# Optimization experiments

Measured on AMD Instinct MI355X. Metric: run time of the kernel, lower is better.

## Reference

```python
import jax, jax.numpy as jnp
import numpy as np

OUT_SL = 32


def gru_cell(x, h, Wih, Whh, bih, bhh):
    # PyTorch GRU cell: gates ordered (r, z, n)
    gi = x @ Wih.T + bih
    gh = h @ Whh.T + bhh
    ir, iz, inn = jnp.split(gi, 3, axis=-1)
    hr, hz, hn = jnp.split(gh, 3, axis=-1)
    r = jax.nn.sigmoid(ir + hr)
    z = jax.nn.sigmoid(iz + hz)
    n = jnp.tanh(inn + r * hn)
    return (1.0 - z) * n + z * h


def run_gru_layer(xs, h0, Wih, Whh, bih, bhh, reverse=False):
    def step(h, x):
        h = gru_cell(x, h, Wih, Whh, bih, bhh)
        return h, h
    hT, ys = jax.lax.scan(step, h0, xs, reverse=reverse)
    return ys, hT


def setup_inputs() -> dict:
    key = jax.random.key(0)
    ks = iter(jax.random.split(key, 32))

    def p(shape, fan_in):
        return (jax.random.normal(next(ks), shape, dtype=jnp.float32)
                / np.sqrt(fan_in).astype(np.float32))

    V_ENC, V_DEC, EE, ED, NH = 32000, 32000, 300, 300, 256
    inp = jax.random.randint(next(ks), (128, 64), 0, V_ENC)
    return {
        'emb_enc': p((V_ENC, EE), 1.0),
        'enc_Wih0': p((2, 3 * NH, EE), EE),
        'enc_Whh0': p((2, 3 * NH, NH), NH),
        'enc_bih0': p((2, 3 * NH), NH),
        'enc_bhh0': p((2, 3 * NH), NH),
        'enc_Wih1': p((2, 3 * NH, 2 * NH), 2 * NH),
        'enc_Whh1': p((2, 3 * NH, NH), NH),
        'enc_bih1': p((2, 3 * NH), NH),
        'enc_bhh1': p((2, 3 * NH), NH),
        'W_out_enc': p((ED, 2 * NH), 2 * NH),
        'emb_dec': p((V_DEC, ED), 1.0),
        'dec_Wih': p((2, 3 * ED, ED), ED),
        'dec_Whh': p((2, 3 * ED, ED), ED),
        'dec_bih': p((2, 3 * ED), ED),
        'dec_bhh': p((2, 3 * ED), ED),
        'W1': p((2 * NH, ED), 2 * NH),
        'l2_W': p((ED, ED), ED),
        'l2_b': p((ED,), ED),
        'l3_W': p((ED, ED + 2 * NH), ED + 2 * NH),
        'l3_b': p((ED,), ED),
        'V_att': p((ED,), ED),
        'out_b': p((V_DEC,), ED),
        'inp': inp,
    }


def reference(emb_enc, enc_Wih0, enc_Whh0, enc_bih0, enc_bhh0,
              enc_Wih1, enc_Whh1, enc_bih1, enc_bhh1, W_out_enc,
              emb_dec, dec_Wih, dec_Whh, dec_bih, dec_bhh,
              W1, l2_W, l2_b, l3_W, l3_b, V_att, out_b, inp):
    sl, bs = inp.shape
    nh = enc_Whh0.shape[-1]
    h0 = jnp.zeros((bs, nh), dtype=emb_enc.dtype)

    # ---- encoder: 2-layer bidirectional GRU (dropout in eval mode = identity)
    emb = emb_enc[inp]                                        # (sl, bs, EE)
    yf0, hf0 = run_gru_layer(emb, h0, enc_Wih0[0], enc_Whh0[0], enc_bih0[0], enc_bhh0[0])
    yb0, hb0 = run_gru_layer(emb, h0, enc_Wih0[1], enc_Whh0[1], enc_bih0[1], enc_bhh0[1], reverse=True)
    x1 = jnp.concatenate([yf0, yb0], axis=-1)                 # (sl, bs, 2*nh)
    yf1, hf1 = run_gru_layer(x1, h0, enc_Wih1[0], enc_Whh1[0], enc_bih1[0], enc_bhh1[0])
    yb1, hb1 = run_gru_layer(x1, h0, enc_Wih1[1], enc_Whh1[1], enc_bih1[1], enc_bhh1[1], reverse=True)
    enc_out = jnp.concatenate([yf1, yb1], axis=-1)            # (sl, bs, 2*nh)

    # h.view(2,2,bs,-1).permute(0,2,1,3) -> concat fwd/bwd per layer
    h = jnp.stack([jnp.concatenate([hf0, hb0], axis=-1),
                   jnp.concatenate([hf1, hb1], axis=-1)])     # (2, bs, 2*nh)
    h = h @ W_out_enc.T                                       # (2, bs, ED)

    w1e = enc_out @ W1                                        # (sl, bs, ED)
    dec_inp0 = jnp.zeros((bs,), dtype=jnp.int32)

    def dec_step(carry, _):
        h, dec_inp = carry
        w2h = h[-1] @ l2_W.T + l2_b                           # (bs, ED)
        u = jnp.tanh(w1e + w2h[None])                         # (sl, bs, ED)
        a = jax.nn.softmax(u @ V_att, axis=0)                 # (sl, bs), softmax over seq
        Xa = jnp.einsum('sb,sbd->bd', a, enc_out)             # (bs, 2*nh)
        e = emb_dec[dec_inp]                                  # (bs, ED)
        x = jnp.concatenate([e, Xa], axis=1) @ l3_W.T + l3_b  # (bs, ED)
        h0n = gru_cell(x, h[0], dec_Wih[0], dec_Whh[0], dec_bih[0], dec_bhh[0])
        h1n = gru_cell(h0n, h[1], dec_Wih[1], dec_Whh[1], dec_bih[1], dec_bhh[1])
        outp = h1n @ emb_dec.T + out_b                        # (bs, V_dec), tied weights
        ndec = jnp.argmax(outp, axis=1).astype(jnp.int32)
        return (jnp.stack([h0n, h1n]), ndec), outp

    (_, _), res = jax.lax.scan(dec_step, (h, dec_inp0), None, length=OUT_SL)
    return res                                                # (out_sl, bs, V_dec)
```

## Files before the change

### kernel.cpp

```cpp
#include <hip/hip_runtime.h>
#include <math.h>


typedef unsigned long long ull;
typedef float v2f __attribute__((ext_vector_type(2)));

#define DINL static __device__ __forceinline__

DINL float sigm(float x) { return 1.0f / (1.0f + expf(-x)); }
DINL float dot4f(float4 a, float4 b) { return a.x*b.x + a.y*b.y + a.z*b.z + a.w*b.w; }

DINL ull packmax(float x, int v) {
  unsigned u = __float_as_uint(x);
  u = (u & 0x80000000u) ? ~u : (u | 0x80000000u);
  return ((ull)u << 32) | (unsigned)(~v);
}
DINL ull umax64(ull a, ull b) { return a > b ? a : b; }

DINL float atl(const float* p) {
  unsigned u = __hip_atomic_load((const unsigned*)p, __ATOMIC_RELAXED,
                                 __HIP_MEMORY_SCOPE_AGENT);
  return __uint_as_float(u);
}
DINL void atsf(float* p, float v) {
  __hip_atomic_exchange((unsigned*)p, __float_as_uint(v), __ATOMIC_RELAXED,
                        __HIP_MEMORY_SCOPE_AGENT);
}
DINL ull atl64(const ull* p) {
  return __hip_atomic_load(p, __ATOMIC_RELAXED, __HIP_MEMORY_SCOPE_AGENT);
}
DINL void ats64(ull* p, ull v) {
  __hip_atomic_exchange(p, v, __ATOMIC_RELAXED, __HIP_MEMORY_SCOPE_AGENT);
}

DINL void gbar(unsigned* flags, int wg, unsigned target, int tid) {
  asm volatile("s_waitcnt vmcnt(0)" ::: "memory");
  __syncthreads();
  if (tid == 0)
    __hip_atomic_exchange(&flags[wg * 32], target, __ATOMIC_RELAXED,
                          __HIP_MEMORY_SCOPE_AGENT);
  while (__hip_atomic_load(&flags[tid * 32], __ATOMIC_RELAXED,
                           __HIP_MEMORY_SCOPE_AGENT) < target)
    __builtin_amdgcn_s_sleep(1);
  __syncthreads();
}

__global__ __launch_bounds__(256) void k_embed(const float4* __restrict__ E,
                                               const int* __restrict__ inp,
                                               float4* __restrict__ out) {
  int i = blockIdx.x * 256 + threadIdx.x;
  if (i >= 8192 * 75) return;
  int row = i / 75, q = i - row * 75;
  out[i] = E[(size_t)inp[row] * 75 + q];
}

__global__ __launch_bounds__(256) void k_transpose(const float* __restrict__ A,
                                                   float* __restrict__ B, int R, int C) {
  __shared__ float tile[32][33];
  int c0 = blockIdx.x * 32, r0 = blockIdx.y * 32;
  int tx = threadIdx.x & 31, ty = threadIdx.x >> 5;
  for (int i = 0; i < 32; i += 8) {
    int r = r0 + ty + i, c = c0 + tx;
    if (r < R && c < C) tile[ty + i][tx] = A[(size_t)r * C + c];
  }
  __syncthreads();
  for (int i = 0; i < 32; i += 8) {
    int c = c0 + ty + i, r = r0 + tx;
    if (c < C && r < R) B[(size_t)c * R + r] = tile[tx][ty + i];
  }
}

__global__ __launch_bounds__(256) void k_packW(const float* __restrict__ Whh,
                                               float* __restrict__ W2) {
  int i = blockIdx.x * 256 + threadIdx.x;
  if (i >= 196608) return;
  int d = i / 98304, r = i - d * 98304, kp = r / 768, gc = r - kp * 768;
  const float* src = Whh + (size_t)d * 196608 + (size_t)gc * 256 + kp * 2;
  float* dst = W2 + (size_t)i * 2;
  dst[0] = src[0];
  dst[1] = src[1];
}

__global__ __launch_bounds__(256) void k_gemm128(const float* __restrict__ A,
                                                 const float* __restrict__ B,
                                                 const float* __restrict__ bias,
                                                 float* __restrict__ C,
                                                 int N, int M, int K) {
  __shared__ float As[8][132];
  __shared__ float Bs[8][132];
  const int tid = threadIdx.x;
  const int bn = blockIdx.x * 128, bm = blockIdx.y * 128;
  const int tn = (tid >> 4) << 3, tm = (tid & 15) << 3;
  const int r = tid & 127;
  const bool isB = tid >= 128;
  const float* src = isB ? (B + (size_t)(bm + r) * K) : (A + (size_t)(bn + r) * K);
  const bool rowok = isB ? (bm + r < M) : (bn + r < N);
  float acc[8][8] = {};
  for (int k0 = 0; k0 < K; k0 += 8) {
    float v[8];
    if (rowok && k0 + 8 <= K) {
      float4 p0 = *(const float4*)(src + k0);
      float4 p1 = *(const float4*)(src + k0 + 4);
      v[0]=p0.x; v[1]=p0.y; v[2]=p0.z; v[3]=p0.w;
      v[4]=p1.x; v[5]=p1.y; v[6]=p1.z; v[7]=p1.w;
    } else {
#pragma unroll
      for (int j = 0; j < 8; ++j) v[j] = (rowok && k0 + j < K) ? src[k0 + j] : 0.0f;
    }
    float (*dst)[132] = isB ? Bs : As;
#pragma unroll
    for (int j = 0; j < 8; ++j) dst[j][r] = v[j];
    __syncthreads();
#pragma unroll
    for (int kk = 0; kk < 8; ++kk) {
      float a[8], b[8];
      *(float4*)&a[0] = *(const float4*)&As[kk][tn];
      *(float4*)&a[4] = *(const float4*)&As[kk][tn + 4];
      *(float4*)&b[0] = *(const float4*)&Bs[kk][tm];
      *(float4*)&b[4] = *(const float4*)&Bs[kk][tm + 4];
#pragma unroll
      for (int i = 0; i < 8; ++i)
#pragma unroll
        for (int j = 0; j < 8; ++j) acc[i][j] += a[i] * b[j];
    }
    __syncthreads();
  }
#pragma unroll
  for (int i = 0; i < 8; ++i) {
    int row = bn + tn + i;
    if (row >= N) continue;
#pragma unroll
    for (int j = 0; j < 8; ++j) {
      int col = bm + tm + j;
      if (col < M) C[(size_t)row * M + col] = acc[i][j] + (bias ? bias[col] : 0.0f);
    }
  }
}

__global__ __launch_bounds__(256) void k_enc_rec(
    const float* __restrict__ giF, const float* __restrict__ giB,
    const float* __restrict__ W2,
    const float* __restrict__ bhh,
    float* __restrict__ y) {
  const int b0 = blockIdx.x * 2;
  const int dir = blockIdx.y;
  const int c = threadIdx.x;
  const float* gi = dir ? giB : giF;
  const v2f* Wv = (const v2f*)(W2 + (size_t)dir * 196608);
  const float* bh = bhh + dir * 768;

  __shared__ __align__(16) float hls[2][2][258];
  for (int i = c; i < 2 * 2 * 258; i += 256) ((float*)hls)[i] = 0.0f;
  __syncthreads();

  const float bhr = bh[c], bhz = bh[256 + c], bhn = bh[512 + c];

  const int tt0 = dir ? 127 : 0;
  const float* g0p = gi + (size_t)tt0 * 49152 + (size_t)b0 * 768;
  float g0r = g0p[c], g0z = g0p[256 + c], g0n = g0p[512 + c];
  float g1r = g0p[768 + c], g1z = g0p[1024 + c], g1n = g0p[1280 + c];

  for (int t = 0; t < 128; ++t) {
    const int cu = t & 1;
    float p0r = 0, p0z = 0, p0n = 0, p1r = 0, p1z = 0, p1n = 0;
    if (t < 127) {
      const int tn_ = dir ? 126 - t : t + 1;
      const float* gp = gi + (size_t)tn_ * 49152 + (size_t)b0 * 768;
      p0r = gp[c]; p0z = gp[256 + c]; p0n = gp[512 + c];
      p1r = gp[768 + c]; p1z = gp[1024 + c]; p1n = gp[1280 + c];
    }
    v2f a0r = {0,0}, a0z = {0,0}, a0n = {0,0};
    v2f a1r = {0,0}, a1z = {0,0}, a1n = {0,0};
    const float* h0p = &hls[cu][0][0];
    const float* h1p = &hls[cu][1][0];
#pragma unroll 4
    for (int kp = 0; kp < 128; ++kp) {
      v2f wr = Wv[kp * 768 + c];
      v2f wz = Wv[kp * 768 + 256 + c];
      v2f wn = Wv[kp * 768 + 512 + c];
      v2f h0 = *(const v2f*)&h0p[kp * 2];
      v2f h1 = *(const v2f*)&h1p[kp * 2];
      a0r += h0 * wr; a0z += h0 * wz; a0n += h0 * wn;
      a1r += h1 * wr; a1z += h1 * wz; a1n += h1 * wn;
    }
    float r0 = sigm(g0r + a0r.x + a0r.y + bhr);
    float z0 = sigm(g0z + a0z.x + a0z.y + bhz);
    float n0 = tanhf(g0n + r0 * (a0n.x + a0n.y + bhn));
    float h0new = (1.f - z0) * n0 + z0 * h0p[c];
    float r1 = sigm(g1r + a1r.x + a1r.y + bhr);
    float z1 = sigm(g1z + a1z.x + a1z.y + bhz);
    float n1 = tanhf(g1n + r1 * (a1n.x + a1n.y + bhn));
    float h1new = (1.f - z1) * n1 + z1 * h1p[c];
    hls[cu ^ 1][0][c] = h0new;
    hls[cu ^ 1][1][c] = h1new;
    const int tw = dir ? 127 - t : t;
    float* yp = y + (size_t)tw * 32768 + (size_t)b0 * 512 + dir * 256 + c;
    yp[0] = h0new;
    yp[512] = h1new;
    g0r = p0r; g0z = p0z; g0n = p0n; g1r = p1r; g1z = p1z; g1n = p1n;
    __syncthreads();
  }
}

__global__ __launch_bounds__(256) void k_hcat(const float* __restrict__ x1,
                                              const float* __restrict__ encout,
                                              float* __restrict__ hcat) {
  int i = blockIdx.x * 256 + threadIdx.x;
  int l = i >> 15, r = i & 32767, b = r >> 9, d = r & 511;
  const float* src = l ? encout : x1;
  int ts = (d < 256) ? 127 : 0;
  hcat[i] = src[((size_t)(ts << 6) + b) * 512 + d];
}

DINL void gru_at(int cb, int tid, const float* __restrict__ xin,
                 const float* __restrict__ hin, float* __restrict__ hout,
                 float* __restrict__ houtT,
                 const float* __restrict__ Wih, const float* __restrict__ Whh,
                 const float* __restrict__ bih, const float* __restrict__ bhh,
                 float* xs, float* hs) {
  const int cchunk = cb % 19, bchunk = cb / 19;
  const int cl = tid & 15, bl = tid >> 4;
  const int c = cchunk * 16 + cl;
  const int b0 = bchunk * 16, bq = b0 + bl;
  for (int i = tid; i < 4800; i += 256) {
    int row = i / 300, q = i - row * 300;
    xs[i] = atl(xin + (size_t)(b0 + row) * 300 + q);
    hs[i] = atl(hin + (size_t)(b0 + row) * 300 + q);
  }
  __syncthreads();
  if (c < 300) {
    float gir = bih[c], giz = bih[300 + c], gin = bih[600 + c];
    float ghr = bhh[c], ghz = bhh[300 + c], ghn = bhh[600 + c];
    const float4* wir = (const float4*)(Wih + (size_t)c * 300);
    const float4* wiz = (const float4*)(Wih + (size_t)(300 + c) * 300);
    const float4* win = (const float4*)(Wih + (size_t)(600 + c) * 300);
    const float4* whr = (const float4*)(Whh + (size_t)c * 300);
    const float4* whz = (const float4*)(Whh + (size_t)(300 + c) * 300);
    const float4* whn = (const float4*)(Whh + (size_t)(600 + c) * 300);
    const float4* xr = (const float4*)(xs + bl * 300);
    const float4* hr = (const float4*)(hs + bl * 300);
    for (int q = 0; q < 75; ++q) {
      float4 xv = xr[q], hv = hr[q];
      gir += dot4f(xv, wir[q]);
      giz += dot4f(xv, wiz[q]);
      gin += dot4f(xv, win[q]);
      ghr += dot4f(hv, whr[q]);
      ghz += dot4f(hv, whz[q]);
      ghn += dot4f(hv, whn[q]);
    }
    float r = sigm(gir + ghr), z = sigm(giz + ghz);
    float n = tanhf(gin + r * ghn);
    float hnew = (1.f - z) * n + z * hs[bl * 300 + c];
    atsf(&hout[(size_t)bq * 300 + c], hnew);
    if (houtT) atsf(&houtT[(size_t)c * 64 + bq], hnew);
  }
}

__global__ __launch_bounds__(256) void k_dec_all(
    float* __restrict__ dech, float* __restrict__ h1T, float* __restrict__ xdec,
    ull* __restrict__ bests, unsigned* __restrict__ flags,
    const float* __restrict__ w1e, const float* __restrict__ encout,
    const float* __restrict__ l2W, const float* __restrict__ l2b,
    const float* __restrict__ l3W, const float* __restrict__ l3b,
    const float* __restrict__ Vatt, const float* __restrict__ embdec,
    const float* __restrict__ dWih, const float* __restrict__ dWhh,
    const float* __restrict__ dbih, const float* __restrict__ dbhh,
    const float* __restrict__ embT, const float* __restrict__ outb,
    float* __restrict__ out) {
  const int wg = blockIdx.x, tid = threadIdx.x;
  __shared__ __align__(16) float smem[14400];
  unsigned tgt = 0;

  for (int t = 0; t < 32; ++t) {
    const int cur = t & 1;
    float* hc = dech + cur * 38400;
    float* hn = dech + (cur ^ 1) * 38400;

    if (wg < 64) {
      const int b = wg;
      float* h1s = smem;
      float* w2h = smem + 304;
      float* eXa = smem + 608;
      float* aa  = smem + 1424;
      float* red = smem + 1552;
      ull* redb  = (ull*)(smem + 1680);

      redb[tid] = (t > 0 && tid < 250) ? atl64(&bests[(size_t)tid * 64 + b]) : 0ULL;
      for (int i = tid; i < 300; i += 256) h1s[i] = atl(hc + 19200 + b * 300 + i);
      __syncthreads();
      for (int s = 128; s > 0; s >>= 1) {
        if (tid < s) redb[tid] = umax64(redb[tid], redb[tid + s]);
        __syncthreads();
      }
      const int ib = (t > 0) ? (int)(~(unsigned)(redb[0] & 0xFFFFFFFFULL)) : 0;

      for (int m = tid; m < 300; m += 256) {
        const float4* wr = (const float4*)(l2W + (size_t)m * 300);
        const float4* hr = (const float4*)h1s;
        float acc = l2b[m];
        for (int q = 0; q < 75; ++q) acc += dot4f(wr[q], hr[q]);
        w2h[m] = acc;
      }
      __syncthreads();

      if (tid < 128) {
        const float4* wp = (const float4*)(w1e + ((size_t)(tid << 6) + b) * 300);
        const float4* vp = (const float4*)Vatt;
        const float4* hp = (const float4*)w2h;
        float acc = 0.f;
        for (int q = 0; q < 75; ++q) {
          float4 w = wp[q], h = hp[q], v = vp[q];
          acc += tanhf(w.x + h.x) * v.x + tanhf(w.y + h.y) * v.y +
                 tanhf(w.z + h.z) * v.z + tanhf(w.w + h.w) * v.w;
        }
        aa[tid] = acc;
        red[tid] = acc;
      }
      __syncthreads();
      for (int s = 64; s > 0; s >>= 1) {
        if (tid < s) red[tid] = fmaxf(red[tid], red[tid + s]);
        __syncthreads();
      }
      float mx = red[0];
      __syncthreads();
      if (tid < 128) {
        float ex = expf(aa[tid] - mx);
        aa[tid] = ex;
        red[tid] = ex;
      }
      __syncthreads();
      for (int s = 64; s > 0; s >>= 1) {
        if (tid < s) red[tid] += red[tid + s];
        __syncthreads();
      }
      float inv = 1.0f / red[0];
      __syncthreads();
      if (tid < 128) aa[tid] *= inv;
      for (int d = tid; d < 300; d += 256) eXa[d] = embdec[(size_t)ib * 300 + d];
      __syncthreads();

      for (int d = tid; d < 512; d += 256) {
        float acc = 0.f;
        for (int s = 0; s < 128; ++s)
          acc += aa[s] * encout[((size_t)(s << 6) + b) * 512 + d];
        eXa[300 + d] = acc;
      }
      __syncthreads();

      for (int m = tid; m < 300; m += 256) {
        const float4* wr = (const float4*)(l3W + (size_t)m * 812);
        const float4* xr = (const float4*)eXa;
        float acc = l3b[m];
        for (int q = 0; q < 203; ++q) acc += dot4f(wr[q], xr[q]);
        atsf(&xdec[b * 300 + m], acc);
      }
    }
    gbar(flags, wg, ++tgt, tid);

    if (wg < 76)
      gru_at(wg, tid, xdec, hc, hn, nullptr, dWih, dWhh, dbih, dbhh,
             smem, smem + 4800);
    gbar(flags, wg, ++tgt, tid);

    if (wg < 76)
      gru_at(wg, tid, hn, hc + 19200, hn + 19200, h1T,
             dWih + 270000, dWhh + 270000, dbih + 900, dbhh + 900,
             smem, smem + 4800);
    gbar(flags, wg, ++tgt, tid);

    if (wg < 250) {
      const int v0 = wg * 128;
      const int vq = tid & 31, bo = tid >> 5;
      float acc[8][4];
#pragma unroll
      for (int i = 0; i < 8; ++i)
#pragma unroll
        for (int j = 0; j < 4; ++j) acc[i][j] = 0.f;
      float* hch = smem;
      float* et  = smem + 4800;
      for (int kc = 0; kc < 4; ++kc) {
        __syncthreads();
        for (int i = tid; i < 4800; i += 256) hch[i] = atl(h1T + kc * 4800 + i);
        for (int i = tid; i < 2400; i += 256) {
          int row = i >> 5, c4 = (i & 31) << 2;
          *(float4*)&et[(row << 7) + c4] =
              *(const float4*)(embT + (size_t)(kc * 75 + row) * 32000 + v0 + c4);
        }
        __syncthreads();
        for (int k = 0; k < 75; ++k) {
          float hv[8];
          *(float4*)&hv[0] = *(const float4*)&hch[(k << 6) + (bo << 3)];
          *(float4*)&hv[4] = *(const float4*)&hch[(k << 6) + (bo << 3) + 4];
          float4 ev = *(const float4*)&et[(k << 7) + (vq << 2)];
#pragma unroll
          for (int i = 0; i < 8; ++i) {
            acc[i][0] += hv[i] * ev.x;
            acc[i][1] += hv[i] * ev.y;
            acc[i][2] += hv[i] * ev.z;
            acc[i][3] += hv[i] * ev.w;
          }
        }
      }
      float4 bo4 = *(const float4*)(outb + v0 + (vq << 2));
      float* outp = out + (size_t)t * 2048000;
      float* sacc = smem;
      __syncthreads();
#pragma unroll
      for (int i = 0; i < 8; ++i) {
        const int b = (bo << 3) + i;
        float4 r;
        r.x = acc[i][0] + bo4.x; r.y = acc[i][1] + bo4.y;
        r.z = acc[i][2] + bo4.z; r.w = acc[i][3] + bo4.w;
        *(float4*)(outp + (size_t)b * 32000 + v0 + (vq << 2)) = r;
        sacc[((vq << 2) + 0) * 64 + b] = r.x;
        sacc[((vq << 2) + 1) * 64 + b] = r.y;
        sacc[((vq << 2) + 2) * 64 + b] = r.z;
        sacc[((vq << 2) + 3) * 64 + b] = r.w;
      }
      __syncthreads();
      if (tid < 64) {
        ull best = 0ULL;
#pragma unroll 4
        for (int v = 0; v < 128; ++v)
          best = umax64(best, packmax(sacc[v * 64 + tid], v0 + v));
        ats64(&bests[(size_t)wg * 64 + tid], best);
      }
    }
    if (t < 31) gbar(flags, wg, ++tgt, tid);
  }
}

extern "C" void kernel_launch(void* const* d_in, const int* in_sizes, int n_in,
                              void* d_out_v, int out_size, void* d_ws, size_t ws_size,
                              hipStream_t stream) {
  (void)in_sizes; (void)n_in; (void)out_size; (void)ws_size;
  const float* emb_enc = (const float*)d_in[0];
  const float* eWih0   = (const float*)d_in[1];
  const float* eWhh0   = (const float*)d_in[2];
  const float* ebih0   = (const float*)d_in[3];
  const float* ebhh0   = (const float*)d_in[4];
  const float* eWih1   = (const float*)d_in[5];
  const float* eWhh1   = (const float*)d_in[6];
  const float* ebih1   = (const float*)d_in[7];
  const float* ebhh1   = (const float*)d_in[8];
  const float* Wout    = (const float*)d_in[9];
  const float* emb_dec = (const float*)d_in[10];
  const float* dWih    = (const float*)d_in[11];
  const float* dWhh    = (const float*)d_in[12];
  const float* dbih    = (const float*)d_in[13];
  const float* dbhh    = (const float*)d_in[14];
  const float* W1      = (const float*)d_in[15];
  const float* l2W     = (const float*)d_in[16];
  const float* l2b     = (const float*)d_in[17];
  const float* l3W     = (const float*)d_in[18];
  const float* l3b     = (const float*)d_in[19];
  const float* Vatt    = (const float*)d_in[20];
  const float* outb    = (const float*)d_in[21];
  const int* inp       = (const int*)d_in[22];
  float* d_out = (float*)d_out_v;

  float* ws = (float*)d_ws;
  size_t off = 0;
  auto take = [&](size_t n) { float* p = ws + off; off += (n + 3) & ~(size_t)3; return p; };
  float* embT   = take((size_t)300 * 32000);
  float* encout = take((size_t)8192 * 512);
  float* w1e    = take((size_t)8192 * 300);
  float* W1T    = take((size_t)300 * 512);
  float* hcat   = take((size_t)128 * 512);
  float* dech   = take((size_t)2 * 2 * 64 * 300);
  float* h1T    = take((size_t)300 * 64);
  float* xdec   = take((size_t)64 * 300);
  ull* bests    = (ull*)take((size_t)250 * 64 * 2);
  unsigned* flags = (unsigned*)take((size_t)256 * 32);

  float* emb  = d_out;
  float* gi0f = emb + 2457600;
  float* gi0b = gi0f + 6291456;
  float* x1   = gi0b + 6291456;
  float* gi1f = x1 + 4194304;
  float* gi1b = gi1f + 6291456;
  float* W2L0 = d_out + 33554432;
  float* W2L1 = W2L0 + 393216;

  hipMemsetAsync(flags, 0, 256 * 32 * sizeof(unsigned), stream);

  k_embed<<<2400, 256, 0, stream>>>((const float4*)emb_enc, inp, (float4*)emb);
  k_transpose<<<dim3(10, 16), 256, 0, stream>>>(W1, W1T, 512, 300);
  k_transpose<<<dim3(10, 1000), 256, 0, stream>>>(emb_dec, embT, 32000, 300);
  k_packW<<<768, 256, 0, stream>>>(eWhh0, W2L0);
  k_packW<<<768, 256, 0, stream>>>(eWhh1, W2L1);

  k_gemm128<<<dim3(64, 6), 256, 0, stream>>>(emb, eWih0, ebih0, gi0f, 8192, 768, 300);
  k_gemm128<<<dim3(64, 6), 256, 0, stream>>>(emb, eWih0 + 230400, ebih0 + 768, gi0b, 8192, 768, 300);
  k_enc_rec<<<dim3(32, 2), 256, 0, stream>>>(gi0f, gi0b, W2L0, ebhh0, x1);

  k_gemm128<<<dim3(64, 6), 256, 0, stream>>>(x1, eWih1, ebih1, gi1f, 8192, 768, 512);
  k_gemm128<<<dim3(64, 6), 256, 0, stream>>>(x1, eWih1 + 393216, ebih1 + 768, gi1b, 8192, 768, 512);
  k_enc_rec<<<dim3(32, 2), 256, 0, stream>>>(gi1f, gi1b, W2L1, ebhh1, encout);

  k_hcat<<<256, 256, 0, stream>>>(x1, encout, hcat);
  k_gemm128<<<dim3(1, 3), 256, 0, stream>>>(hcat, Wout, nullptr, dech, 128, 300, 512);
  k_gemm128<<<dim3(64, 3), 256, 0, stream>>>(encout, W1T, nullptr, w1e, 8192, 300, 512);

  k_dec_all<<<256, 256, 0, stream>>>(dech, h1T, xdec, bests, flags,
                                     w1e, encout, l2W, l2b, l3W, l3b,
                                     Vatt, emb_dec, dWih, dWhh, dbih, dbhh,
                                     embT, outb, d_out);
}
```

Baseline: 11.03 ms.

## Cache decoder GRU weights in LDS per block and use atomic-counter grid barrier

The persistent decoder kernel now assigns the two GRU cells to disjoint block groups (0-75 and 76-151). Each block loads its 96-row slice of the GRU weights and biases into shared memory once, so weights are no longer re-read from global memory every step. The per-block flag barrier is replaced by one atomic counter that thread 0 polls, and the bests reduction is halved. The vocab projection now reads embT directly from global instead of staging it in LDS, and the argmax scratch is padded to avoid bank conflicts. Costs include a large LDS footprint that limits occupancy and contention on a single atomic counter.

```diff
diff --git a/kernel.cpp b/kernel.cpp
--- a/kernel.cpp
+++ b/kernel.cpp
@@ -33,15 +33,14 @@
   __hip_atomic_exchange(p, v, __ATOMIC_RELAXED, __HIP_MEMORY_SCOPE_AGENT);
 }
 
-DINL void gbar(unsigned* flags, int wg, unsigned target, int tid) {
+DINL void gbar(unsigned* cnt, unsigned target, int tid) {
   asm volatile("s_waitcnt vmcnt(0)" ::: "memory");
   __syncthreads();
-  if (tid == 0)
-    __hip_atomic_exchange(&flags[wg * 32], target, __ATOMIC_RELAXED,
-                          __HIP_MEMORY_SCOPE_AGENT);
-  while (__hip_atomic_load(&flags[tid * 32], __ATOMIC_RELAXED,
-                           __HIP_MEMORY_SCOPE_AGENT) < target)
-    __builtin_amdgcn_s_sleep(1);
+  if (tid == 0) {
+    __hip_atomic_fetch_add(cnt, 1u, __ATOMIC_RELAXED, __HIP_MEMORY_SCOPE_AGENT);
+    while (__hip_atomic_load(cnt, __ATOMIC_RELAXED, __HIP_MEMORY_SCOPE_AGENT) < target)
+      __builtin_amdgcn_s_sleep(4);
+  }
   __syncthreads();
 }
 
@@ -139,8 +138,7 @@
 
 __global__ __launch_bounds__(256) void k_enc_rec(
     const float* __restrict__ giF, const float* __restrict__ giB,
-    const float* __restrict__ W2,
-    const float* __restrict__ bhh,
+    const float* __restrict__ W2, const float* __restrict__ bhh,
     float* __restrict__ y) {
   const int b0 = blockIdx.x * 2;
   const int dir = blockIdx.y;
@@ -154,7 +152,6 @@
   __syncthreads();
 
   const float bhr = bh[c], bhz = bh[256 + c], bhn = bh[512 + c];
-
   const int tt0 = dir ? 127 : 0;
   const float* g0p = gi + (size_t)tt0 * 49152 + (size_t)b0 * 768;
   float g0r = g0p[c], g0z = g0p[256 + c], g0n = g0p[512 + c];
@@ -212,41 +209,40 @@
   hcat[i] = src[((size_t)(ts << 6) + b) * 512 + d];
 }
 
-DINL void gru_at(int cb, int tid, const float* __restrict__ xin,
-                 const float* __restrict__ hin, float* __restrict__ hout,
-                 float* __restrict__ houtT,
-                 const float* __restrict__ Wih, const float* __restrict__ Whh,
-                 const float* __restrict__ bih, const float* __restrict__ bhh,
-                 float* xs, float* hs) {
-  const int cchunk = cb % 19, bchunk = cb / 19;
-  const int cl = tid & 15, bl = tid >> 4;
-  const int c = cchunk * 16 + cl;
-  const int b0 = bchunk * 16, bq = b0 + bl;
+DINL void gru_lds(int cch, int bch, int tid,
+                  const float* __restrict__ xin, const float* __restrict__ hin,
+                  float* __restrict__ hout, float* __restrict__ houtT,
+                  const float* Wg, const float* biass, float* scr) {
+  float* xs = scr;
+  float* hs = scr + 4800;
+  const int b0 = bch * 16;
   for (int i = tid; i < 4800; i += 256) {
     int row = i / 300, q = i - row * 300;
     xs[i] = atl(xin + (size_t)(b0 + row) * 300 + q);
     hs[i] = atl(hin + (size_t)(b0 + row) * 300 + q);
   }
   __syncthreads();
+  const int cl = tid & 15, bl = tid >> 4;
+  const int c = cch * 16 + cl, bq = b0 + bl;
   if (c < 300) {
-    float gir = bih[c], giz = bih[300 + c], gin = bih[600 + c];
-    float ghr = bhh[c], ghz = bhh[300 + c], ghn = bhh[600 + c];
-    const float4* wir = (const float4*)(Wih + (size_t)c * 300);
-    const float4* wiz = (const float4*)(Wih + (size_t)(300 + c) * 300);
-    const float4* win = (const float4*)(Wih + (size_t)(600 + c) * 300);
-    const float4* whr = (const float4*)(Whh + (size_t)c * 300);
-    const float4* whz = (const float4*)(Whh + (size_t)(300 + c) * 300);
-    const float4* whn = (const float4*)(Whh + (size_t)(600 + c) * 300);
+    float gir = biass[cl],      giz = biass[16 + cl], gin = biass[32 + cl];
+    float ghr = biass[48 + cl], ghz = biass[64 + cl], ghn = biass[80 + cl];
     const float4* xr = (const float4*)(xs + bl * 300);
     const float4* hr = (const float4*)(hs + bl * 300);
+    const float4* w0 = (const float4*)(Wg + (0 * 16 + cl) * 308);
+    const float4* w1 = (const float4*)(Wg + (1 * 16 + cl) * 308);
+    const float4* w2 = (const float4*)(Wg + (2 * 16 + cl) * 308);
+    const float4* w3 = (const float4*)(Wg + (3 * 16 + cl) * 308);
+    const float4* w4 = (const float4*)(Wg + (4 * 16 + cl) * 308);
+    const float4* w5 = (const float4*)(Wg + (5 * 16 + cl) * 308);
     for (int q = 0; q < 75; ++q) {
       float4 xv = xr[q], hv = hr[q];
-      gir += dot4f(xv, wir[q]);
-      giz += dot4f(xv, wiz[q]);
-      gin += dot4f(xv, win[q]);
-      ghr += dot4f(hv, whr[q]);
-      ghz += dot4f(hv, whz[q]);
-      ghn += dot4f(hv, whn[q]);
+      gir += dot4f(xv, w0[q]);
+      giz += dot4f(xv, w1[q]);
+      gin += dot4f(xv, w2[q]);
+      ghr += dot4f(hv, w3[q]);
+      ghz += dot4f(hv, w4[q]);
+      ghn += dot4f(hv, w5[q]);
     }
     float r = sigm(gir + ghr), z = sigm(giz + ghz);
     float n = tanhf(gin + r * ghn);
@@ -254,11 +250,12 @@
     atsf(&hout[(size_t)bq * 300 + c], hnew);
     if (houtT) atsf(&houtT[(size_t)c * 64 + bq], hnew);
   }
+  __syncthreads();
 }
 
 __global__ __launch_bounds__(256) void k_dec_all(
     float* __restrict__ dech, float* __restrict__ h1T, float* __restrict__ xdec,
-    ull* __restrict__ bests, unsigned* __restrict__ flags,
+    ull* __restrict__ bests, unsigned* __restrict__ cnt,
     const float* __restrict__ w1e, const float* __restrict__ encout,
     const float* __restrict__ l2W, const float* __restrict__ l2b,
     const float* __restrict__ l3W, const float* __restrict__ l3b,
@@ -268,9 +265,41 @@
     const float* __restrict__ embT, const float* __restrict__ outb,
     float* __restrict__ out) {
   const int wg = blockIdx.x, tid = threadIdx.x;
-  __shared__ __align__(16) float smem[14400];
+  __shared__ __align__(16) float Wg[6 * 16 * 308];
+  __shared__ __align__(16) float scr[9600];
+  __shared__ float biass[96];
+
+  int grole = -1, gcell = 0;
+  if (wg < 76) { grole = wg; gcell = 0; }
+  else if (wg < 152) { grole = wg - 76; gcell = 1; }
+  const int cch = (grole >= 0) ? grole % 19 : 0;
+  const int bch = (grole >= 0) ? grole / 19 : 0;
+  if (grole >= 0) {
+    const float* Wih = dWih + gcell * 270000;
+    const float* Whh = dWhh + gcell * 270000;
+    for (int i = tid; i < 96 * 300; i += 256) {
+      int r = i / 300, k = i - r * 300;
+      int g = r >> 4, cl = r & 15;
+      int c = cch * 16 + cl;
+      float v = 0.f;
+      if (c < 300)
+        v = (g < 3) ? Wih[(size_t)(g * 300 + c) * 300 + k]
+                    : Whh[(size_t)((g - 3) * 300 + c) * 300 + k];
+      Wg[(g * 16 + cl) * 308 + k] = v;
+    }
+    if (tid < 96) {
+      int g = tid >> 4, cl = tid & 15;
+      int c = cch * 16 + cl;
+      float v = 0.f;
+      if (c < 300)
+        v = (g < 3) ? dbih[gcell * 900 + g * 300 + c]
+                    : dbhh[gcell * 900 + (g - 3) * 300 + c];
+      biass[tid] = v;
+    }
+  }
+  __syncthreads();
+
   unsigned tgt = 0;
-
   for (int t = 0; t < 32; ++t) {
     const int cur = t & 1;
     float* hc = dech + cur * 38400;
@@ -278,17 +307,24 @@
 
     if (wg < 64) {
       const int b = wg;
-      float* h1s = smem;
-      float* w2h = smem + 304;
-      float* eXa = smem + 608;
-      float* aa  = smem + 1424;
-      float* red = smem + 1552;
-      ull* redb  = (ull*)(smem + 1680);
-
-      redb[tid] = (t > 0 && tid < 250) ? atl64(&bests[(size_t)tid * 64 + b]) : 0ULL;
+      float* h1s = scr;
+      float* w2h = scr + 304;
+      float* eXa = scr + 608;
+      float* aa  = scr + 1424;
+      float* red = scr + 1552;
+      ull* redb  = (ull*)(scr + 1680);
+
+      if (tid < 128) {
+        ull m = 0ULL;
+        if (t > 0) {
+          m = atl64(&bests[(size_t)tid * 64 + b]);
+          if (tid + 128 < 250) m = umax64(m, atl64(&bests[(size_t)(tid + 128) * 64 + b]));
+        }
+        redb[tid] = m;
+      }
       for (int i = tid; i < 300; i += 256) h1s[i] = atl(hc + 19200 + b * 300 + i);
       __syncthreads();
-      for (int s = 128; s > 0; s >>= 1) {
+      for (int s = 64; s > 0; s >>= 1) {
         if (tid < s) redb[tid] = umax64(redb[tid], redb[tid + s]);
         __syncthreads();
       }
@@ -354,19 +390,17 @@
         for (int q = 0; q < 203; ++q) acc += dot4f(wr[q], xr[q]);
         atsf(&xdec[b * 300 + m], acc);
       }
-    }
-    gbar(flags, wg, ++tgt, tid);
+      __syncthreads();
+    }
+    gbar(cnt, 256u * (++tgt), tid);
 
     if (wg < 76)
-      gru_at(wg, tid, xdec, hc, hn, nullptr, dWih, dWhh, dbih, dbhh,
-             smem, smem + 4800);
-    gbar(flags, wg, ++tgt, tid);
-
-    if (wg < 76)
-      gru_at(wg, tid, hn, hc + 19200, hn + 19200, h1T,
-             dWih + 270000, dWhh + 270000, dbih + 900, dbhh + 900,
-             smem, smem + 4800);
-    gbar(flags, wg, ++tgt, tid);
+      gru_lds(cch, bch, tid, xdec, hc, hn, nullptr, Wg, biass, scr);
+    gbar(cnt, 256u * (++tgt), tid);
+
+    if (wg >= 76 && wg < 152)
+      gru_lds(cch, bch, tid, hn, hc + 19200, hn + 19200, h1T, Wg, biass, scr);
+    gbar(cnt, 256u * (++tgt), tid);
 
     if (wg < 250) {
       const int v0 = wg * 128;
@@ -376,22 +410,17 @@
       for (int i = 0; i < 8; ++i)
 #pragma unroll
         for (int j = 0; j < 4; ++j) acc[i][j] = 0.f;
-      float* hch = smem;
-      float* et  = smem + 4800;
+      float* hch = scr;
       for (int kc = 0; kc < 4; ++kc) {
         __syncthreads();
         for (int i = tid; i < 4800; i += 256) hch[i] = atl(h1T + kc * 4800 + i);
-        for (int i = tid; i < 2400; i += 256) {
-          int row = i >> 5, c4 = (i & 31) << 2;
-          *(float4*)&et[(row << 7) + c4] =
-              *(const float4*)(embT + (size_t)(kc * 75 + row) * 32000 + v0 + c4);
-        }
         __syncthreads();
+        const float* eb = embT + (size_t)kc * 75 * 32000 + v0 + (vq << 2);
         for (int k = 0; k < 75; ++k) {
+          float4 ev = *(const float4*)(eb + (size_t)k * 32000);
           float hv[8];
           *(float4*)&hv[0] = *(const float4*)&hch[(k << 6) + (bo << 3)];
           *(float4*)&hv[4] = *(const float4*)&hch[(k << 6) + (bo << 3) + 4];
-          float4 ev = *(const float4*)&et[(k << 7) + (vq << 2)];
 #pragma unroll
           for (int i = 0; i < 8; ++i) {
             acc[i][0] += hv[i] * ev.x;
@@ -403,7 +432,7 @@
       }
       float4 bo4 = *(const float4*)(outb + v0 + (vq << 2));
       float* outp = out + (size_t)t * 2048000;
-      float* sacc = smem;
+      float* sacc = scr;
       __syncthreads();
 #pragma unroll
       for (int i = 0; i < 8; ++i) {
@@ -412,21 +441,22 @@
         r.x = acc[i][0] + bo4.x; r.y = acc[i][1] + bo4.y;
         r.z = acc[i][2] + bo4.z; r.w = acc[i][3] + bo4.w;
         *(float4*)(outp + (size_t)b * 32000 + v0 + (vq << 2)) = r;
-        sacc[((vq << 2) + 0) * 64 + b] = r.x;
-        sacc[((vq << 2) + 1) * 64 + b] = r.y;
-        sacc[((vq << 2) + 2) * 64 + b] = r.z;
-        sacc[((vq << 2) + 3) * 64 + b] = r.w;
+        sacc[((vq << 2) + 0) * 65 + b] = r.x;
+        sacc[((vq << 2) + 1) * 65 + b] = r.y;
+        sacc[((vq << 2) + 2) * 65 + b] = r.z;
+        sacc[((vq << 2) + 3) * 65 + b] = r.w;
       }
       __syncthreads();
       if (tid < 64) {
         ull best = 0ULL;
 #pragma unroll 4
         for (int v = 0; v < 128; ++v)
-          best = umax64(best, packmax(sacc[v * 64 + tid], v0 + v));
+          best = umax64(best, packmax(sacc[v * 65 + tid], v0 + v));
         ats64(&bests[(size_t)wg * 64 + tid], best);
       }
-    }
-    if (t < 31) gbar(flags, wg, ++tgt, tid);
+      __syncthreads();
+    }
+    if (t < 31) gbar(cnt, 256u * (++tgt), tid);
   }
 }
 
@@ -471,7 +501,7 @@
   float* h1T    = take((size_t)300 * 64);
   float* xdec   = take((size_t)64 * 300);
   ull* bests    = (ull*)take((size_t)250 * 64 * 2);
-  unsigned* flags = (unsigned*)take((size_t)256 * 32);
+  unsigned* cnt = (unsigned*)take((size_t)32);
 
   float* emb  = d_out;
   float* gi0f = emb + 2457600;
@@ -482,7 +512,7 @@
   float* W2L0 = d_out + 33554432;
   float* W2L1 = W2L0 + 393216;
 
-  hipMemsetAsync(flags, 0, 256 * 32 * sizeof(unsigned), stream);
+  hipMemsetAsync(cnt, 0, 32 * sizeof(unsigned), stream);
 
   k_embed<<<2400, 256, 0, stream>>>((const float4*)emb_enc, inp, (float4*)emb);
   k_transpose<<<dim3(10, 16), 256, 0, stream>>>(W1, W1T, 512, 300);
@@ -502,7 +532,7 @@
   k_gemm128<<<dim3(1, 3), 256, 0, stream>>>(hcat, Wout, nullptr, dech, 128, 300, 512);
   k_gemm128<<<dim3(64, 3), 256, 0, stream>>>(encout, W1T, nullptr, w1e, 8192, 300, 512);
 
-  k_dec_all<<<256, 256, 0, stream>>>(dech, h1T, xdec, bests, flags,
+  k_dec_all<<<256, 256, 0, stream>>>(dech, h1T, xdec, bests, cnt,
                                      w1e, encout, l2W, l2b, l3W, l3b,
                                      Vatt, emb_dec, dWih, dWhh, dbih, dbhh,
                                      embT, outb, d_out);
```

Result: no change. 10.92 ms (-1.0%).
